# Kernel optimization log

Measured on AMD Instinct MI355X. Metric: run time of the kernel, lower is better.

Reference implementation:

```python
import jax, jax.numpy as jnp
import numpy as np

N_NODES = 50000
N_EDGES = 800000
NEG_SLOPE = 0.2


def gat_conv(x, src, dst, W, att_src, att_dst, bias, heads, out_ch, concat):
    """PyG-style GATConv (eval mode, self-loops already included in src/dst)."""
    N = x.shape[0]
    h = (x @ W).reshape(N, heads, out_ch)                      # [N,H,C]
    a_src = (h * att_src).sum(-1)                              # [N,H]
    a_dst = (h * att_dst).sum(-1)                              # [N,H]
    alpha = jax.nn.leaky_relu(a_src[src] + a_dst[dst], NEG_SLOPE)  # [E,H]
    # numerically stable segment softmax over incoming edges of each dst node
    amax = jax.ops.segment_max(alpha, dst, num_segments=N)     # [N,H]
    amax = jax.lax.stop_gradient(jnp.where(jnp.isfinite(amax), amax, 0.0))
    ex = jnp.exp(alpha - amax[dst])                            # [E,H]
    denom = jax.ops.segment_sum(ex, dst, num_segments=N)       # [N,H]
    coef = ex / (denom[dst] + 1e-16)                           # [E,H]
    msg = h[src] * coef[..., None]                             # [E,H,C]
    out = jax.ops.segment_sum(msg, dst, num_segments=N)        # [N,H,C]
    out = out.reshape(N, heads * out_ch) if concat else out.mean(axis=1)
    return out + bias


def setup_inputs() -> dict:
    key = jax.random.key(0)
    ks = jax.random.split(key, 12)
    x = jax.random.normal(ks[0], (N_NODES, 2), dtype=jnp.float32)
    edge_index = jax.random.randint(ks[1], (2, N_EDGES), 0, N_NODES, dtype=jnp.int64)
    # layer1: 2 -> 32, heads=4, concat
    W1 = jax.random.normal(ks[2], (2, 4 * 32), dtype=jnp.float32) * 0.5
    att_src1 = jax.random.normal(ks[3], (1, 4, 32), dtype=jnp.float32) * 0.1
    att_dst1 = jax.random.normal(ks[4], (1, 4, 32), dtype=jnp.float32) * 0.1
    b1 = jax.random.normal(ks[5], (128,), dtype=jnp.float32) * 0.01
    # layer2: 128 -> 128, heads=1, concat=False
    W2 = jax.random.normal(ks[6], (128, 128), dtype=jnp.float32) * (1.0 / np.sqrt(128.0))
    att_src2 = jax.random.normal(ks[7], (1, 1, 128), dtype=jnp.float32) * 0.1
    att_dst2 = jax.random.normal(ks[8], (1, 1, 128), dtype=jnp.float32) * 0.1
    b2 = jax.random.normal(ks[9], (128,), dtype=jnp.float32) * 0.01
    return {"x": x, "edge_index": edge_index, "W1": W1, "att_src1": att_src1,
            "att_dst1": att_dst1, "b1": b1, "W2": W2, "att_src2": att_src2,
            "att_dst2": att_dst2, "b2": b2}


def reference(x, edge_index, W1, att_src1, att_dst1, b1, W2, att_src2, att_dst2, b2):
    N = x.shape[0]
    loops = jnp.arange(N, dtype=edge_index.dtype)
    src = jnp.concatenate([edge_index[0], loops])  # PyG add_self_loops=True
    dst = jnp.concatenate([edge_index[1], loops])
    h = gat_conv(x, src, dst, W1, att_src1, att_dst1, b1, 4, 32, True)
    h = jax.nn.relu(h)
    h = gat_conv(h, src, dst, W2, att_src2, att_dst2, b2, 1, 128, False)
    # global_mean_pool with a single graph (batch all zeros) then squeeze(0)
    return h.mean(axis=0)  # [128]
```

## Files before the change

### kernel.cpp

```cpp
#include <hip/hip_runtime.h>

#define NN 50000
#define NE 800000
#define ET (NE + NN)
#define EPW 4096
#define NWGP ((ET + EPW - 1) / EPW)
#define NB 196
#define BCAP 6144
#define RC 8

typedef unsigned short u16;
typedef unsigned int u32;
typedef unsigned char u8;

__device__ __forceinline__ float lrelu(float a) { return a > 0.f ? a : 0.2f * a; }

__global__ void k_init(u32* __restrict__ bcur, u32* __restrict__ bcur2,
                       u32* __restrict__ ovf, u32* __restrict__ ovf2,
                       float* __restrict__ z,
                       const float* __restrict__ W1, const float* __restrict__ as1,
                       const float* __restrict__ ad1, const float* __restrict__ W2,
                       const float* __restrict__ as2, const float* __restrict__ ad2,
                       float* __restrict__ AD, float* __restrict__ vs,
                       float* __restrict__ vd) {
    int i = blockIdx.x * blockDim.x + threadIdx.x;
    if (i < 256) { bcur[i] = 0; bcur2[i] = 0; }
    if (i == 0)  { *ovf = 0; *ovf2 = 0; }
    if (i < 128) {
        z[i] = 0.f;
        float a = 0.f, d = 0.f;
        for (int c = 0; c < 128; ++c) {
            float wv = W2[i * 128 + c];
            a = fmaf(wv, as2[c], a);
            d = fmaf(wv, ad2[c], d);
        }
        vs[i] = a; vd[i] = d;
    }
    if (i >= 128 && i < 144) {
        int q = i - 128, isD = q >> 3, j = (q >> 2) & 1, hd = q & 3;
        const float* att = isD ? ad1 : as1;
        float acc = 0.f;
        for (int ch = 0; ch < 32; ++ch)
            acc = fmaf(W1[j * 128 + hd * 32 + ch], att[hd * 32 + ch], acc);
        AD[isD * 8 + j * 4 + hd] = acc;
    }
}

__global__ __launch_bounds__(256) void k_part(
        const int* __restrict__ ei,
        u32* __restrict__ bcur, u32* __restrict__ bcur2,
        u32* __restrict__ stg, u32* __restrict__ stg_s,
        u32* __restrict__ stg2, u32* __restrict__ stg2s,
        u32* __restrict__ ovf, u32* __restrict__ ovf2) {
    __shared__ u32 lcnt[256], sc[256], lbase[256], gbase[256];
    __shared__ u32 lpair[EPW];
    __shared__ u8  lbkt[EPW];
    int t = threadIdx.x;
    int e0 = blockIdx.x * EPW;

    u32 pr[16]; bool vd_[16]; u16 rk[16]; u8 bk[16];
#pragma unroll
    for (int j = 0; j < 16; ++j) {
        int e = e0 + j * 256 + t;
        vd_[j] = (e < ET);
        if (vd_[j]) {
            int s, d;
            if (e < NE) { s = ei[e]; d = ei[NE + e]; } else { s = d = e - NE; }
            pr[j] = ((u32)d << 16) | (u32)s;
        }
    }
    lcnt[t] = 0;
    __syncthreads();
#pragma unroll
    for (int j = 0; j < 16; ++j) if (vd_[j]) {
        int b = pr[j] >> 24;
        bk[j] = (u8)b;
        rk[j] = (u16)atomicAdd(&lcnt[b], 1u);
    }
    __syncthreads();
    u32 v = lcnt[t];
    sc[t] = v;
    __syncthreads();
#pragma unroll
    for (int st = 1; st < 256; st <<= 1) {
        u32 u = (t >= st) ? sc[t - st] : 0;
        __syncthreads();
        sc[t] += u;
        __syncthreads();
    }
    lbase[t] = sc[t] - v;
    gbase[t] = atomicAdd(&bcur[t], v);
    __syncthreads();
#pragma unroll
    for (int j = 0; j < 16; ++j) if (vd_[j]) {
        u32 idx = lbase[bk[j]] + rk[j];
        lpair[idx] = pr[j];
        lbkt[idx]  = bk[j];
    }
    __syncthreads();
    int nloc = lbase[255] + lcnt[255];
    for (int i = t; i < nloc; i += 256) {
        u32 b = lbkt[i];
        u32 g = gbase[b] + (i - lbase[b]);
        u32 p = lpair[i];
        if (g < BCAP) stg[(size_t)b * BCAP + g] = p;
        else { u32 o = atomicAdd(ovf, 1u); if (o < 4096) stg2[o] = p; }
    }
    __syncthreads();
    lcnt[t] = 0;
    __syncthreads();
#pragma unroll
    for (int j = 0; j < 16; ++j) if (vd_[j]) {
        int b = (pr[j] & 0xFFFFu) >> 8;
        bk[j] = (u8)b;
        rk[j] = (u16)atomicAdd(&lcnt[b], 1u);
    }
    __syncthreads();
    v = lcnt[t];
    sc[t] = v;
    __syncthreads();
#pragma unroll
    for (int st = 1; st < 256; st <<= 1) {
        u32 u = (t >= st) ? sc[t - st] : 0;
        __syncthreads();
        sc[t] += u;
        __syncthreads();
    }
    lbase[t] = sc[t] - v;
    gbase[t] = atomicAdd(&bcur2[t], v);
    __syncthreads();
#pragma unroll
    for (int j = 0; j < 16; ++j) if (vd_[j]) {
        u32 p2 = (pr[j] << 16) | (pr[j] >> 16);
        u32 idx = lbase[bk[j]] + rk[j];
        lpair[idx] = p2;
        lbkt[idx]  = bk[j];
    }
    __syncthreads();
    nloc = lbase[255] + lcnt[255];
    for (int i = t; i < nloc; i += 256) {
        u32 b = lbkt[i];
        u32 g = gbase[b] + (i - lbase[b]);
        u32 p = lpair[i];
        if (g < BCAP) stg_s[(size_t)b * BCAP + g] = p;
        else { u32 o = atomicAdd(ovf2, 1u); if (o < 4096) stg2s[o] = p; }
    }
}

__global__ __launch_bounds__(256) void k_scanb(
        const u32* __restrict__ bcur, u32* __restrict__ bbase,
        const u32* __restrict__ bcur2, u32* __restrict__ bbase2,
        int* __restrict__ off, int* __restrict__ off_s) {
    __shared__ u32 sh[256];
    int t = threadIdx.x;
    u32 v = (t < NB) ? bcur[t] : 0;
    sh[t] = v;
    __syncthreads();
#pragma unroll
    for (int s = 1; s < 256; s <<= 1) {
        u32 u = (t >= s) ? sh[t - s] : 0;
        __syncthreads();
        sh[t] += u;
        __syncthreads();
    }
    if (t < NB) bbase[t] = sh[t] - v;
    __syncthreads();
    u32 v2 = (t < NB) ? bcur2[t] : 0;
    sh[t] = v2;
    __syncthreads();
#pragma unroll
    for (int s = 1; s < 256; s <<= 1) {
        u32 u = (t >= s) ? sh[t - s] : 0;
        __syncthreads();
        sh[t] += u;
        __syncthreads();
    }
    if (t < NB) bbase2[t] = sh[t] - v2;
    if (t == 0) { off[NN] = ET; off_s[NN] = ET; }
}

__global__ __launch_bounds__(256) void k_place(
        const u32* __restrict__ bbase, const u32* __restrict__ bcur,
        const u32* __restrict__ stg, const u32* __restrict__ stg2,
        const u32* __restrict__ ovf,
        int* __restrict__ off, u16* __restrict__ out16) {
    __shared__ u32 hist[256], sc[256], lcur[256];
    __shared__ u16 lcsr[BCAP];
    int b = blockIdx.x, t = threadIdx.x;
    int n0 = b << 8;
    int S0 = (int)bbase[b];
    u32 cnt = bcur[b];
    hist[t] = 0;
    __syncthreads();
    u32 cmain = min(cnt, (u32)BCAP);
    for (u32 i = t; i < cmain; i += 256)
        atomicAdd(&hist[(stg[(size_t)b * BCAP + i] >> 16) & 255u], 1u);
    if (cnt > cmain) {
        u32 no = min(*ovf, 4096u);
        for (u32 i = t; i < no; i += 256) {
            u32 p = stg2[i];
            if ((p >> 24) == (u32)b) atomicAdd(&hist[(p >> 16) & 255u], 1u);
        }
    }
    __syncthreads();
    u32 v = hist[t];
    sc[t] = v;
    __syncthreads();
#pragma unroll
    for (int s = 1; s < 256; s <<= 1) {
        u32 u = (t >= s) ? sc[t - s] : 0;
        __syncthreads();
        sc[t] += u;
        __syncthreads();
    }
    u32 lexcl = sc[t] - v;
    int n = n0 + t;
    if (n < NN) off[n] = S0 + (int)lexcl;
    lcur[t] = lexcl;
    __syncthreads();
    bool direct = (cnt > (u32)BCAP);
    for (u32 i = t; i < cmain; i += 256) {
        u32 p = stg[(size_t)b * BCAP + i];
        u32 r = atomicAdd(&lcur[(p >> 16) & 255u], 1u);
        if (direct) out16[S0 + r] = (u16)(p & 0xFFFFu);
        else        lcsr[r] = (u16)(p & 0xFFFFu);
    }
    if (cnt > cmain) {
        u32 no = min(*ovf, 4096u);
        for (u32 i = t; i < no; i += 256) {
            u32 p = stg2[i];
            if ((p >> 24) == (u32)b) {
                u32 r = atomicAdd(&lcur[(p >> 16) & 255u], 1u);
                if (direct) out16[S0 + r] = (u16)(p & 0xFFFFu);
                else        lcsr[r] = (u16)(p & 0xFFFFu);
            }
        }
    }
    __syncthreads();
    if (!direct)
        for (u32 i = t; i < cnt; i += 256) out16[S0 + i] = lcsr[i];
}

__global__ __launch_bounds__(128) void k_agg1x(
        const int* __restrict__ off, const u16* __restrict__ csr,
        const float* __restrict__ x, const float* __restrict__ AD,
        const float* __restrict__ W1, const float* __restrict__ b1,
        const float* __restrict__ vs, const float* __restrict__ vd,
        float* __restrict__ x2, float* __restrict__ asrc2,
        float* __restrict__ adst2) {
    int t = threadIdx.x;
    int wv = t >> 6, l = t & 63;
    int n = blockIdx.x * 2 + wv;
    if (n >= NN) return;
    int hd = l >> 4, li = l & 15;
    int e0 = off[n], deg = off[n + 1] - e0;
    float2 xd = *(const float2*)(x + 2 * n);
    float A0 = AD[hd], A1 = AD[4 + hd], D0 = AD[8 + hd], D1 = AD[12 + hd];
    float adn = fmaf(D0, xd.x, D1 * xd.y);

    float den = 0.f, S0 = 0.f, S1 = 0.f;
    if (deg <= 16 * RC) {
        float xx[RC], xy[RC], al[RC];
#pragma unroll
        for (int i = 0; i < RC; ++i) {
            int e = li + i * 16;
            if (e < deg) {
                int s = csr[e0 + e];
                float2 xv = *(const float2*)(x + 2 * s);
                xx[i] = xv.x; xy[i] = xv.y;
                al[i] = lrelu(fmaf(A0, xv.x, A1 * xv.y) + adn);
            } else {
                xx[i] = 0.f; xy[i] = 0.f; al[i] = -1e30f;
            }
        }
        float mymax = -1e30f;
#pragma unroll
        for (int i = 0; i < RC; ++i) mymax = fmaxf(mymax, al[i]);
#pragma unroll
        for (int m = 8; m >= 1; m >>= 1) mymax = fmaxf(mymax, __shfl_xor(mymax, m));
#pragma unroll
        for (int i = 0; i < RC; ++i) {
            float ex = __expf(al[i] - mymax);
            den += ex;
            S0 = fmaf(ex, xx[i], S0);
            S1 = fmaf(ex, xy[i], S1);
        }
    } else {
        float mymax = -1e30f;
        for (int e = li; e < deg; e += 16) {
            int s = csr[e0 + e];
            float2 xv = *(const float2*)(x + 2 * s);
            mymax = fmaxf(mymax, lrelu(fmaf(A0, xv.x, A1 * xv.y) + adn));
        }
#pragma unroll
        for (int m = 8; m >= 1; m >>= 1) mymax = fmaxf(mymax, __shfl_xor(mymax, m));
        for (int e = li; e < deg; e += 16) {
            int s = csr[e0 + e];
            float2 xv = *(const float2*)(x + 2 * s);
            float ex = __expf(lrelu(fmaf(A0, xv.x, A1 * xv.y) + adn) - mymax);
            den += ex;
            S0 = fmaf(ex, xv.x, S0);
            S1 = fmaf(ex, xv.y, S1);
        }
    }
#pragma unroll
    for (int m = 8; m >= 1; m >>= 1) {
        den += __shfl_xor(den, m);
        S0  += __shfl_xor(S0, m);
        S1  += __shfl_xor(S1, m);
    }
    float inv = 1.f / (den + 1e-16f);

    int c0 = 2 * l;
    float o0 = (S0 * W1[c0]     + S1 * W1[128 + c0])     * inv;
    float o1 = (S0 * W1[c0 + 1] + S1 * W1[128 + c0 + 1]) * inv;
    float v0 = fmaxf(o0 + b1[c0], 0.f);
    float v1 = fmaxf(o1 + b1[c0 + 1], 0.f);
    *(float2*)(x2 + (size_t)n * 128 + c0) = make_float2(v0, v1);

    float ps = fmaf(v0, vs[c0], v1 * vs[c0 + 1]);
    float pd = fmaf(v0, vd[c0], v1 * vd[c0 + 1]);
#pragma unroll
    for (int m = 32; m >= 1; m >>= 1) {
        ps += __shfl_xor(ps, m);
        pd += __shfl_xor(pd, m);
    }
    if (l == 0) { asrc2[n] = ps; adst2[n] = pd; }
}

__global__ __launch_bounds__(128) void k_den(
        const int* __restrict__ off, const u16* __restrict__ csr,
        const float* __restrict__ asrc2, const float* __restrict__ adst2,
        float2* __restrict__ mxinv) {
    int t = threadIdx.x;
    int g = t >> 4, li = t & 15;
    int n = blockIdx.x * 8 + g;
    if (n >= NN) return;
    int e0 = off[n], deg = off[n + 1] - e0;
    float adn = adst2[n];
    float mymax = -1e30f, den = 0.f;
    if (deg <= 16 * RC) {
        float al[RC];
#pragma unroll
        for (int i = 0; i < RC; ++i) {
            int e = li + i * 16;
            al[i] = (e < deg) ? lrelu(asrc2[csr[e0 + e]] + adn) : -1e30f;
        }
#pragma unroll
        for (int i = 0; i < RC; ++i) mymax = fmaxf(mymax, al[i]);
#pragma unroll
        for (int m = 8; m >= 1; m >>= 1) mymax = fmaxf(mymax, __shfl_xor(mymax, m));
#pragma unroll
        for (int i = 0; i < RC; ++i) den += __expf(al[i] - mymax);
    } else {
        for (int e = li; e < deg; e += 16)
            mymax = fmaxf(mymax, lrelu(asrc2[csr[e0 + e]] + adn));
#pragma unroll
        for (int m = 8; m >= 1; m >>= 1) mymax = fmaxf(mymax, __shfl_xor(mymax, m));
        for (int e = li; e < deg; e += 16)
            den += __expf(lrelu(asrc2[csr[e0 + e]] + adn) - mymax);
    }
#pragma unroll
    for (int m = 8; m >= 1; m >>= 1) den += __shfl_xor(den, m);
    if (li == 0) mxinv[n] = make_float2(mymax, 1.f / (den + 1e-16f));
}

__global__ __launch_bounds__(128) void k_wgath(
        const int* __restrict__ off_s, const u16* __restrict__ csc,
        const float* __restrict__ asrc2, const float* __restrict__ adst2,
        const float2* __restrict__ mxinv, float* __restrict__ w) {
    int t = threadIdx.x;
    int g = t >> 4, li = t & 15;
    int n = blockIdx.x * 8 + g;
    if (n >= NN) return;
    int e0 = off_s[n], deg = off_s[n + 1] - e0;
    float as = asrc2[n];
    float acc = 0.f;
    if (deg <= 16 * RC) {
#pragma unroll
        for (int i = 0; i < RC; ++i) {
            int e = li + i * 16;
            if (e < deg) {
                int d = csc[e0 + e];
                float2 mi = mxinv[d];
                acc += __expf(lrelu(as + adst2[d]) - mi.x) * mi.y;
            }
        }
    } else {
        for (int e = li; e < deg; e += 16) {
            int d = csc[e0 + e];
            float2 mi = mxinv[d];
            acc += __expf(lrelu(as + adst2[d]) - mi.x) * mi.y;
        }
    }
#pragma unroll
    for (int m = 8; m >= 1; m >>= 1) acc += __shfl_xor(acc, m);
    if (li == 0) w[n] = acc;
}

__global__ __launch_bounds__(256) void k_wsum(const float* __restrict__ w,
                                              const float* __restrict__ x2,
                                              float* __restrict__ z) {
    __shared__ float red[256];
    int t = threadIdx.x, c = t & 127, rp = t >> 7;
    float acc = 0.f;
    for (int n = blockIdx.x * 2 + rp; n < NN; n += 2048)
        acc = fmaf(w[n], x2[(size_t)n * 128 + c], acc);
    red[t] = acc;
    __syncthreads();
    if (t < 128) atomicAdd(z + t, red[t] + red[t + 128]);
}

__global__ __launch_bounds__(128) void k_out(const float* __restrict__ z,
                                             const float* __restrict__ W2,
                                             const float* __restrict__ b2,
                                             float* __restrict__ out) {
    int c = threadIdx.x;
    float acc = 0.f;
    for (int k = 0; k < 128; ++k)
        acc = fmaf(z[k], W2[k * 128 + c], acc);
    out[c] = b2[c] + acc * (1.0f / NN);
}

extern "C" void kernel_launch(void* const* d_in, const int* in_sizes, int n_in,
                              void* d_out, int out_size, void* d_ws, size_t ws_size,
                              hipStream_t stream) {
    const float* x   = (const float*)d_in[0];
    const int*   ei  = (const int*)d_in[1];
    const float* W1  = (const float*)d_in[2];
    const float* as1 = (const float*)d_in[3];
    const float* ad1 = (const float*)d_in[4];
    const float* b1  = (const float*)d_in[5];
    const float* W2  = (const float*)d_in[6];
    const float* as2 = (const float*)d_in[7];
    const float* ad2 = (const float*)d_in[8];
    const float* b2  = (const float*)d_in[9];
    float* out = (float*)d_out;

    char* ws     = (char*)d_ws;
    float* x2    = (float*)ws;
    u32*  stg    = (u32*)x2;
    u32*  stg_s  = stg + (size_t)NB * BCAP;
    float* w     = x2 + (size_t)NN * 128;
    float* asrc2 = w + NN;
    float* adst2 = asrc2 + NN;
    float2* mxinv = (float2*)(adst2 + NN);
    int* off     = (int*)(mxinv + NN);
    int* off_s   = off + NN + 1;
    u32* bcur    = (u32*)(off_s + NN + 1);
    u32* bcur2   = bcur + 256;
    u32* bbase   = bcur2 + 256;
    u32* bbase2  = bbase + 256;
    u32* ovf     = bbase2 + 256;
    u32* ovf2    = ovf + 4;
    u32* stg2    = ovf2 + 4;
    u32* stg2s   = stg2 + 4096;
    u16* csr16   = (u16*)(stg2s + 4096);
    u16* csc16   = csr16 + ET;
    float* AD    = (float*)(csc16 + ET);
    float* vs    = AD + 16;
    float* vd    = vs + 128;
    float* z     = vd + 128;

    k_init<<<(NN + 255) / 256, 256, 0, stream>>>(bcur, bcur2, ovf, ovf2, z,
                                                 W1, as1, ad1, W2, as2, ad2,
                                                 AD, vs, vd);
    k_part<<<NWGP, 256, 0, stream>>>(ei, bcur, bcur2, stg, stg_s,
                                     stg2, stg2s, ovf, ovf2);
    k_scanb<<<1, 256, 0, stream>>>(bcur, bbase, bcur2, bbase2, off, off_s);
    k_place<<<NB, 256, 0, stream>>>(bbase, bcur, stg, stg2, ovf, off, csr16);
    k_place<<<NB, 256, 0, stream>>>(bbase2, bcur2, stg_s, stg2s, ovf2, off_s, csc16);

    k_agg1x<<<(NN + 1) / 2, 128, 0, stream>>>(off, csr16, x, AD, W1, b1,
                                              vs, vd, x2, asrc2, adst2);
    k_den<<<(NN + 7) / 8, 128, 0, stream>>>(off, csr16, asrc2, adst2, mxinv);
    k_wgath<<<(NN + 7) / 8, 128, 0, stream>>>(off_s, csc16, asrc2, adst2, mxinv, w);
    k_wsum<<<1024, 256, 0, stream>>>(w, x2, z);
    k_out<<<1, 128, 0, stream>>>(z, W2, b2, out);
}
```

Before: 144.4 us.

## Fuse aggregation stages into one cooperative kernel with grid syncs

```diff
diff --git a/kernel.cpp b/kernel.cpp
--- a/kernel.cpp
+++ b/kernel.cpp
@@ -1,4 +1,5 @@
 #include <hip/hip_runtime.h>
+#include <hip/hip_cooperative_groups.h>
 
 #define NN 50000
 #define NE 800000
@@ -7,25 +8,27 @@
 #define NWGP ((ET + EPW - 1) / EPW)
 #define NB 196
 #define BCAP 6144
-#define RC 8
+#define CG 1024
 
 typedef unsigned short u16;
 typedef unsigned int u32;
 typedef unsigned char u8;
 
+namespace cg = cooperative_groups;
+
 __device__ __forceinline__ float lrelu(float a) { return a > 0.f ? a : 0.2f * a; }
 
-__global__ void k_init(u32* __restrict__ bcur, u32* __restrict__ bcur2,
-                       u32* __restrict__ ovf, u32* __restrict__ ovf2,
-                       float* __restrict__ z,
-                       const float* __restrict__ W1, const float* __restrict__ as1,
-                       const float* __restrict__ ad1, const float* __restrict__ W2,
-                       const float* __restrict__ as2, const float* __restrict__ ad2,
-                       float* __restrict__ AD, float* __restrict__ vs,
-                       float* __restrict__ vd) {
-    int i = blockIdx.x * blockDim.x + threadIdx.x;
-    if (i < 256) { bcur[i] = 0; bcur2[i] = 0; }
-    if (i == 0)  { *ovf = 0; *ovf2 = 0; }
+__global__ __launch_bounds__(256) void k_init(
+        u32* __restrict__ bcur, u32* __restrict__ bcur2,
+        u32* __restrict__ ovf, u32* __restrict__ ovf2,
+        float* __restrict__ z, int* __restrict__ off, int* __restrict__ off_s,
+        const float* __restrict__ W1, const float* __restrict__ as1,
+        const float* __restrict__ ad1, const float* __restrict__ W2,
+        const float* __restrict__ as2, const float* __restrict__ ad2,
+        float* __restrict__ AD, float* __restrict__ vs, float* __restrict__ vd) {
+    int i = threadIdx.x;
+    bcur[i] = 0; bcur2[i] = 0;
+    if (i == 0) { *ovf = 0; *ovf2 = 0; off[NN] = ET; off_s[NN] = ET; }
     if (i < 128) {
         z[i] = 0.f;
         float a = 0.f, d = 0.f;
@@ -147,14 +150,28 @@
     }
 }
 
-__global__ __launch_bounds__(256) void k_scanb(
-        const u32* __restrict__ bcur, u32* __restrict__ bbase,
-        const u32* __restrict__ bcur2, u32* __restrict__ bbase2,
-        int* __restrict__ off, int* __restrict__ off_s) {
-    __shared__ u32 sh[256];
-    int t = threadIdx.x;
-    u32 v = (t < NB) ? bcur[t] : 0;
-    sh[t] = v;
+__global__ __launch_bounds__(256) void k_place2(
+        const u32* __restrict__ bcurA, const u32* __restrict__ bcurB,
+        const u32* __restrict__ stgA, const u32* __restrict__ stgB,
+        const u32* __restrict__ stg2A, const u32* __restrict__ stg2B,
+        const u32* __restrict__ ovfA, const u32* __restrict__ ovfB,
+        int* __restrict__ offA, int* __restrict__ offB,
+        u16* __restrict__ outA, u16* __restrict__ outB) {
+    __shared__ u32 sh[256], hist[256], sc[256], lcur[256];
+    __shared__ u16 lcsr[BCAP];
+    int blk = blockIdx.x, t = threadIdx.x;
+    bool isB = (blk >= NB);
+    int b = isB ? blk - NB : blk;
+    const u32* bcur = isB ? bcurB : bcurA;
+    const u32* stg  = isB ? stgB  : stgA;
+    const u32* stg2 = isB ? stg2B : stg2A;
+    const u32* ovf  = isB ? ovfB  : ovfA;
+    int* off   = isB ? offB : offA;
+    u16* out16 = isB ? outB : outA;
+
+    u32 vv = (t < NB) ? bcur[t] : 0;
+    sh[t] = vv;
+    hist[t] = 0;
     __syncthreads();
 #pragma unroll
     for (int s = 1; s < 256; s <<= 1) {
@@ -163,36 +180,10 @@
         sh[t] += u;
         __syncthreads();
     }
-    if (t < NB) bbase[t] = sh[t] - v;
-    __syncthreads();
-    u32 v2 = (t < NB) ? bcur2[t] : 0;
-    sh[t] = v2;
-    __syncthreads();
-#pragma unroll
-    for (int s = 1; s < 256; s <<= 1) {
-        u32 u = (t >= s) ? sh[t - s] : 0;
-        __syncthreads();
-        sh[t] += u;
-        __syncthreads();
-    }
-    if (t < NB) bbase2[t] = sh[t] - v2;
-    if (t == 0) { off[NN] = ET; off_s[NN] = ET; }
-}
-
-__global__ __launch_bounds__(256) void k_place(
-        const u32* __restrict__ bbase, const u32* __restrict__ bcur,
-        const u32* __restrict__ stg, const u32* __restrict__ stg2,
-        const u32* __restrict__ ovf,
-        int* __restrict__ off, u16* __restrict__ out16) {
-    __shared__ u32 hist[256], sc[256], lcur[256];
-    __shared__ u16 lcsr[BCAP];
-    int b = blockIdx.x, t = threadIdx.x;
-    int n0 = b << 8;
-    int S0 = (int)bbase[b];
+    int S0 = (int)(sh[b] - bcur[b]);
     u32 cnt = bcur[b];
-    hist[t] = 0;
-    __syncthreads();
     u32 cmain = min(cnt, (u32)BCAP);
+
     for (u32 i = t; i < cmain; i += 256)
         atomicAdd(&hist[(stg[(size_t)b * BCAP + i] >> 16) & 255u], 1u);
     if (cnt > cmain) {
@@ -214,7 +205,7 @@
         __syncthreads();
     }
     u32 lexcl = sc[t] - v;
-    int n = n0 + t;
+    int n = (b << 8) + t;
     if (n < NN) off[n] = S0 + (int)lexcl;
     lcur[t] = lexcl;
     __syncthreads();
@@ -241,185 +232,116 @@
         for (u32 i = t; i < cnt; i += 256) out16[S0 + i] = lcsr[i];
 }
 
-__global__ __launch_bounds__(128) void k_agg1x(
+__global__ __launch_bounds__(256, 4) void k_l2(
         const int* __restrict__ off, const u16* __restrict__ csr,
+        const int* __restrict__ off_s, const u16* __restrict__ csc,
         const float* __restrict__ x, const float* __restrict__ AD,
         const float* __restrict__ W1, const float* __restrict__ b1,
         const float* __restrict__ vs, const float* __restrict__ vd,
+        const float* __restrict__ W2, const float* __restrict__ b2,
         float* __restrict__ x2, float* __restrict__ asrc2,
-        float* __restrict__ adst2) {
+        float* __restrict__ adst2, float* __restrict__ dinv,
+        float* __restrict__ w, float* __restrict__ z,
+        float* __restrict__ out) {
+    cg::grid_group grid = cg::this_grid();
+    __shared__ float red[256];
     int t = threadIdx.x;
-    int wv = t >> 6, l = t & 63;
-    int n = blockIdx.x * 2 + wv;
-    if (n >= NN) return;
-    int hd = l >> 4, li = l & 15;
-    int e0 = off[n], deg = off[n + 1] - e0;
-    float2 xd = *(const float2*)(x + 2 * n);
-    float A0 = AD[hd], A1 = AD[4 + hd], D0 = AD[8 + hd], D1 = AD[12 + hd];
-    float adn = fmaf(D0, xd.x, D1 * xd.y);
-
-    float den = 0.f, S0 = 0.f, S1 = 0.f;
-    if (deg <= 16 * RC) {
-        float xx[RC], xy[RC], al[RC];
-#pragma unroll
-        for (int i = 0; i < RC; ++i) {
-            int e = li + i * 16;
-            if (e < deg) {
+
+    {
+        int wv = t >> 6, l = t & 63;
+        int hd = l >> 4, li = l & 15;
+        float A0 = AD[hd], A1 = AD[4 + hd], D0 = AD[8 + hd], D1 = AD[12 + hd];
+        int c0 = 2 * l;
+        float w1a = W1[c0], w1b = W1[128 + c0];
+        float w1c = W1[c0 + 1], w1d = W1[128 + c0 + 1];
+        float bb0 = b1[c0], bb1 = b1[c0 + 1];
+        float vs0 = vs[c0], vs1 = vs[c0 + 1];
+        float vd0 = vd[c0], vd1 = vd[c0 + 1];
+        for (int n = blockIdx.x * 4 + wv; n < NN; n += CG * 4) {
+            int e0 = off[n], deg = off[n + 1] - e0;
+            float2 xd = *(const float2*)(x + 2 * n);
+            float adn = fmaf(D0, xd.x, D1 * xd.y);
+            float den = 0.f, S0 = 0.f, S1 = 0.f;
+            for (int e = li; e < deg; e += 16) {
                 int s = csr[e0 + e];
                 float2 xv = *(const float2*)(x + 2 * s);
-                xx[i] = xv.x; xy[i] = xv.y;
-                al[i] = lrelu(fmaf(A0, xv.x, A1 * xv.y) + adn);
-            } else {
-                xx[i] = 0.f; xy[i] = 0.f; al[i] = -1e30f;
-            }
-        }
-        float mymax = -1e30f;
-#pragma unroll
-        for (int i = 0; i < RC; ++i) mymax = fmaxf(mymax, al[i]);
-#pragma unroll
-        for (int m = 8; m >= 1; m >>= 1) mymax = fmaxf(mymax, __shfl_xor(mymax, m));
-#pragma unroll
-        for (int i = 0; i < RC; ++i) {
-            float ex = __expf(al[i] - mymax);
-            den += ex;
-            S0 = fmaf(ex, xx[i], S0);
-            S1 = fmaf(ex, xy[i], S1);
-        }
-    } else {
-        float mymax = -1e30f;
-        for (int e = li; e < deg; e += 16) {
-            int s = csr[e0 + e];
-            float2 xv = *(const float2*)(x + 2 * s);
-            mymax = fmaxf(mymax, lrelu(fmaf(A0, xv.x, A1 * xv.y) + adn));
-        }
-#pragma unroll
-        for (int m = 8; m >= 1; m >>= 1) mymax = fmaxf(mymax, __shfl_xor(mymax, m));
-        for (int e = li; e < deg; e += 16) {
-            int s = csr[e0 + e];
-            float2 xv = *(const float2*)(x + 2 * s);
-            float ex = __expf(lrelu(fmaf(A0, xv.x, A1 * xv.y) + adn) - mymax);
-            den += ex;
-            S0 = fmaf(ex, xv.x, S0);
-            S1 = fmaf(ex, xv.y, S1);
-        }
-    }
-#pragma unroll
-    for (int m = 8; m >= 1; m >>= 1) {
-        den += __shfl_xor(den, m);
-        S0  += __shfl_xor(S0, m);
-        S1  += __shfl_xor(S1, m);
-    }
-    float inv = 1.f / (den + 1e-16f);
-
-    int c0 = 2 * l;
-    float o0 = (S0 * W1[c0]     + S1 * W1[128 + c0])     * inv;
-    float o1 = (S0 * W1[c0 + 1] + S1 * W1[128 + c0 + 1]) * inv;
-    float v0 = fmaxf(o0 + b1[c0], 0.f);
-    float v1 = fmaxf(o1 + b1[c0 + 1], 0.f);
-    *(float2*)(x2 + (size_t)n * 128 + c0) = make_float2(v0, v1);
-
-    float ps = fmaf(v0, vs[c0], v1 * vs[c0 + 1]);
-    float pd = fmaf(v0, vd[c0], v1 * vd[c0 + 1]);
-#pragma unroll
-    for (int m = 32; m >= 1; m >>= 1) {
-        ps += __shfl_xor(ps, m);
-        pd += __shfl_xor(pd, m);
-    }
-    if (l == 0) { asrc2[n] = ps; adst2[n] = pd; }
-}
-
-__global__ __launch_bounds__(128) void k_den(
-        const int* __restrict__ off, const u16* __restrict__ csr,
-        const float* __restrict__ asrc2, const float* __restrict__ adst2,
-        float2* __restrict__ mxinv) {
-    int t = threadIdx.x;
-    int g = t >> 4, li = t & 15;
-    int n = blockIdx.x * 8 + g;
-    if (n >= NN) return;
-    int e0 = off[n], deg = off[n + 1] - e0;
-    float adn = adst2[n];
-    float mymax = -1e30f, den = 0.f;
-    if (deg <= 16 * RC) {
-        float al[RC];
-#pragma unroll
-        for (int i = 0; i < RC; ++i) {
-            int e = li + i * 16;
-            al[i] = (e < deg) ? lrelu(asrc2[csr[e0 + e]] + adn) : -1e30f;
-        }
-#pragma unroll
-        for (int i = 0; i < RC; ++i) mymax = fmaxf(mymax, al[i]);
-#pragma unroll
-        for (int m = 8; m >= 1; m >>= 1) mymax = fmaxf(mymax, __shfl_xor(mymax, m));
-#pragma unroll
-        for (int i = 0; i < RC; ++i) den += __expf(al[i] - mymax);
-    } else {
-        for (int e = li; e < deg; e += 16)
-            mymax = fmaxf(mymax, lrelu(asrc2[csr[e0 + e]] + adn));
-#pragma unroll
-        for (int m = 8; m >= 1; m >>= 1) mymax = fmaxf(mymax, __shfl_xor(mymax, m));
-        for (int e = li; e < deg; e += 16)
-            den += __expf(lrelu(asrc2[csr[e0 + e]] + adn) - mymax);
-    }
-#pragma unroll
-    for (int m = 8; m >= 1; m >>= 1) den += __shfl_xor(den, m);
-    if (li == 0) mxinv[n] = make_float2(mymax, 1.f / (den + 1e-16f));
-}
-
-__global__ __launch_bounds__(128) void k_wgath(
-        const int* __restrict__ off_s, const u16* __restrict__ csc,
-        const float* __restrict__ asrc2, const float* __restrict__ adst2,
-        const float2* __restrict__ mxinv, float* __restrict__ w) {
-    int t = threadIdx.x;
-    int g = t >> 4, li = t & 15;
-    int n = blockIdx.x * 8 + g;
-    if (n >= NN) return;
-    int e0 = off_s[n], deg = off_s[n + 1] - e0;
-    float as = asrc2[n];
-    float acc = 0.f;
-    if (deg <= 16 * RC) {
-#pragma unroll
-        for (int i = 0; i < RC; ++i) {
-            int e = li + i * 16;
-            if (e < deg) {
+                float al = lrelu(fmaf(A0, xv.x, A1 * xv.y) + adn);
+                float ex = __expf(fminf(al, 80.f));
+                den += ex;
+                S0 = fmaf(ex, xv.x, S0);
+                S1 = fmaf(ex, xv.y, S1);
+            }
+#pragma unroll
+            for (int m = 8; m >= 1; m >>= 1) {
+                den += __shfl_xor(den, m);
+                S0  += __shfl_xor(S0, m);
+                S1  += __shfl_xor(S1, m);
+            }
+            float inv = 1.f / (den + 1e-16f);
+            float v0 = fmaxf(fmaf(S0, w1a, S1 * w1b) * inv + bb0, 0.f);
+            float v1 = fmaxf(fmaf(S0, w1c, S1 * w1d) * inv + bb1, 0.f);
+            *(float2*)(x2 + (size_t)n * 128 + c0) = make_float2(v0, v1);
+            float ps = fmaf(v0, vs0, v1 * vs1);
+            float pd = fmaf(v0, vd0, v1 * vd1);
+#pragma unroll
+            for (int m = 32; m >= 1; m >>= 1) {
+                ps += __shfl_xor(ps, m);
+                pd += __shfl_xor(pd, m);
+            }
+            if (l == 0) { asrc2[n] = ps; adst2[n] = pd; }
+        }
+    }
+    grid.sync();
+
+    {
+        int g16 = t >> 4, li = t & 15;
+        for (int n = blockIdx.x * 16 + g16; n < NN; n += CG * 16) {
+            int e0 = off[n], deg = off[n + 1] - e0;
+            float adn = adst2[n];
+            float den = 0.f;
+            for (int e = li; e < deg; e += 16)
+                den += __expf(fminf(lrelu(asrc2[csr[e0 + e]] + adn), 80.f));
+#pragma unroll
+            for (int m = 8; m >= 1; m >>= 1) den += __shfl_xor(den, m);
+            if (li == 0) dinv[n] = 1.f / (den + 1e-16f);
+        }
+    }
+    grid.sync();
+
+    {
+        int g16 = t >> 4, li = t & 15;
+        for (int n = blockIdx.x * 16 + g16; n < NN; n += CG * 16) {
+            int e0 = off_s[n], deg = off_s[n + 1] - e0;
+            float as = asrc2[n];
+            float acc = 0.f;
+            for (int e = li; e < deg; e += 16) {
                 int d = csc[e0 + e];
-                float2 mi = mxinv[d];
-                acc += __expf(lrelu(as + adst2[d]) - mi.x) * mi.y;
-            }
-        }
-    } else {
-        for (int e = li; e < deg; e += 16) {
-            int d = csc[e0 + e];
-            float2 mi = mxinv[d];
-            acc += __expf(lrelu(as + adst2[d]) - mi.x) * mi.y;
-        }
-    }
-#pragma unroll
-    for (int m = 8; m >= 1; m >>= 1) acc += __shfl_xor(acc, m);
-    if (li == 0) w[n] = acc;
-}
-
-__global__ __launch_bounds__(256) void k_wsum(const float* __restrict__ w,
-                                              const float* __restrict__ x2,
-                                              float* __restrict__ z) {
-    __shared__ float red[256];
-    int t = threadIdx.x, c = t & 127, rp = t >> 7;
-    float acc = 0.f;
-    for (int n = blockIdx.x * 2 + rp; n < NN; n += 2048)
-        acc = fmaf(w[n], x2[(size_t)n * 128 + c], acc);
-    red[t] = acc;
-    __syncthreads();
-    if (t < 128) atomicAdd(z + t, red[t] + red[t + 128]);
-}
-
-__global__ __launch_bounds__(128) void k_out(const float* __restrict__ z,
-                                             const float* __restrict__ W2,
-                                             const float* __restrict__ b2,
-                                             float* __restrict__ out) {
-    int c = threadIdx.x;
-    float acc = 0.f;
-    for (int k = 0; k < 128; ++k)
-        acc = fmaf(z[k], W2[k * 128 + c], acc);
-    out[c] = b2[c] + acc * (1.0f / NN);
+                acc = fmaf(__expf(fminf(lrelu(as + adst2[d]), 80.f)), dinv[d], acc);
+            }
+#pragma unroll
+            for (int m = 8; m >= 1; m >>= 1) acc += __shfl_xor(acc, m);
+            if (li == 0) w[n] = acc;
+        }
+    }
+    grid.sync();
+
+    {
+        int c = t & 127, rp = t >> 7;
+        float acc = 0.f;
+        for (int n = blockIdx.x * 2 + rp; n < NN; n += CG * 2)
+            acc = fmaf(w[n], x2[(size_t)n * 128 + c], acc);
+        red[t] = acc;
+        __syncthreads();
+        if (t < 128) atomicAdd(z + t, red[t] + red[t + 128]);
+    }
+    grid.sync();
+
+    if (blockIdx.x == 0 && t < 128) {
+        float acc = 0.f;
+        for (int k = 0; k < 128; ++k)
+            acc = fmaf(z[k], W2[k * 128 + t], acc);
+        out[t] = b2[t] + acc * (1.0f / NN);
+    }
 }
 
 extern "C" void kernel_launch(void* const* d_in, const int* in_sizes, int n_in,
@@ -444,14 +366,12 @@
     float* w     = x2 + (size_t)NN * 128;
     float* asrc2 = w + NN;
     float* adst2 = asrc2 + NN;
-    float2* mxinv = (float2*)(adst2 + NN);
-    int* off     = (int*)(mxinv + NN);
+    float* dinv  = adst2 + NN;
+    int* off     = (int*)(dinv + NN);
     int* off_s   = off + NN + 1;
     u32* bcur    = (u32*)(off_s + NN + 1);
     u32* bcur2   = bcur + 256;
-    u32* bbase   = bcur2 + 256;
-    u32* bbase2  = bbase + 256;
-    u32* ovf     = bbase2 + 256;
+    u32* ovf     = bcur2 + 256;
     u32* ovf2    = ovf + 4;
     u32* stg2    = ovf2 + 4;
     u32* stg2s   = stg2 + 4096;
@@ -462,19 +382,18 @@
     float* vd    = vs + 128;
     float* z     = vd + 128;
 
-    k_init<<<(NN + 255) / 256, 256, 0, stream>>>(bcur, bcur2, ovf, ovf2, z,
-                                                 W1, as1, ad1, W2, as2, ad2,
-                                                 AD, vs, vd);
+    k_init<<<1, 256, 0, stream>>>(bcur, bcur2, ovf, ovf2, z, off, off_s,
+                                  W1, as1, ad1, W2, as2, ad2, AD, vs, vd);
     k_part<<<NWGP, 256, 0, stream>>>(ei, bcur, bcur2, stg, stg_s,
                                      stg2, stg2s, ovf, ovf2);
-    k_scanb<<<1, 256, 0, stream>>>(bcur, bbase, bcur2, bbase2, off, off_s);
-    k_place<<<NB, 256, 0, stream>>>(bbase, bcur, stg, stg2, ovf, off, csr16);
-    k_place<<<NB, 256, 0, stream>>>(bbase2, bcur2, stg_s, stg2s, ovf2, off_s, csc16);
-
-    k_agg1x<<<(NN + 1) / 2, 128, 0, stream>>>(off, csr16, x, AD, W1, b1,
-                                              vs, vd, x2, asrc2, adst2);
-    k_den<<<(NN + 7) / 8, 128, 0, stream>>>(off, csr16, asrc2, adst2, mxinv);
-    k_wgath<<<(NN + 7) / 8, 128, 0, stream>>>(off_s, csc16, asrc2, adst2, mxinv, w);
-    k_wsum<<<1024, 256, 0, stream>>>(w, x2, z);
-    k_out<<<1, 128, 0, stream>>>(z, W2, b2, out);
-}
+    k_place2<<<2 * NB, 256, 0, stream>>>(bcur, bcur2, stg, stg_s,
+                                         stg2, stg2s, ovf, ovf2,
+                                         off, off_s, csr16, csc16);
+    void* args[] = {(void*)&off, (void*)&csr16, (void*)&off_s, (void*)&csc16,
+                    (void*)&x, (void*)&AD, (void*)&W1, (void*)&b1,
+                    (void*)&vs, (void*)&vd, (void*)&W2, (void*)&b2,
+                    (void*)&x2, (void*)&asrc2, (void*)&adst2, (void*)&dinv,
+                    (void*)&w, (void*)&z, (void*)&out};
+    hipLaunchCooperativeKernel((const void*)k_l2, dim3(CG), dim3(256),
+                               args, 0, stream);
+}
```

After: 564.2 us. 3.91x slower.
